# Kernel tuning notes

Hardware: AMD Instinct MI355X
Metric: run time of the kernel (lower is better)

The kernel has to match this reference:

```python
import jax, jax.numpy as jnp
import numpy as np

N_NODES = 50000
N_EDGES = 800000
D_IN = 128
D_HID = 128
D_OUT = 128


def _graph_conv(x, src, dst, ew, w_rel, w_root, b):
    # PyG GraphConv: out_i = (sum_{j->i} ew_ji * x_j) @ w_rel.T + b + x_i @ w_root.T
    msg = x[src] * ew[:, None]                                   # [E, F] gather + scale
    agg = jax.ops.segment_sum(msg, dst, num_segments=x.shape[0])  # [N, F] scatter-add
    return agg @ w_rel.T + x @ w_root.T + b


def setup_inputs() -> dict:
    key = jax.random.key(0)
    ks = jax.random.split(key, 12)
    s = 0.05
    x = jax.random.normal(ks[0], (N_NODES, D_IN), dtype=jnp.float32)
    edge_index = jax.random.randint(ks[1], (2, N_EDGES), 0, N_NODES, dtype=jnp.int32)
    edge_weight = jax.random.uniform(ks[2], (N_EDGES,), dtype=jnp.float32)
    return {
        "x": x,
        "edge_index": edge_index,
        "edge_weight": edge_weight,
        "w1_rel": jax.random.normal(ks[3], (D_HID, D_IN), dtype=jnp.float32) * s,
        "w1_root": jax.random.normal(ks[4], (D_HID, D_IN), dtype=jnp.float32) * s,
        "b1": jnp.zeros((D_HID,), dtype=jnp.float32),
        "w2_rel": jax.random.normal(ks[5], (D_HID, D_HID), dtype=jnp.float32) * s,
        "w2_root": jax.random.normal(ks[6], (D_HID, D_HID), dtype=jnp.float32) * s,
        "b2": jnp.zeros((D_HID,), dtype=jnp.float32),
        "w3_rel": jax.random.normal(ks[7], (D_OUT, D_HID), dtype=jnp.float32) * s,
        "w3_root": jax.random.normal(ks[8], (D_OUT, D_HID), dtype=jnp.float32) * s,
        "b3": jnp.zeros((D_OUT,), dtype=jnp.float32),
    }


def reference(x, edge_index, edge_weight,
              w1_rel, w1_root, b1,
              w2_rel, w2_root, b2,
              w3_rel, w3_root, b3):
    src, dst = edge_index[0], edge_index[1]
    h = _graph_conv(x, src, dst, edge_weight, w1_rel, w1_root, b1)
    h = jax.nn.relu(h)  # dropout is identity in eval mode
    h = _graph_conv(h, src, dst, edge_weight, w2_rel, w2_root, b2)
    h = jax.nn.relu(h)
    out = _graph_conv(h, src, dst, edge_weight, w3_rel, w3_root, b3)
    return out
```

## Files before the change

kernel.cpp:

```cpp
#include <hip/hip_runtime.h>
#include <hip/hip_bf16.h>

#define DFEAT   128
#define BCAP    2048
#define NB_MAX  1024

typedef __attribute__((ext_vector_type(8))) short bf16x8;
typedef __attribute__((ext_vector_type(4))) float f32x4;
typedef unsigned int uint;


__global__ __launch_bounds__(1024) void bin_scatter(const int* __restrict__ src,
                                                    const int* __restrict__ dst,
                                                    const float* __restrict__ ew,
                                                    int* __restrict__ cursor,
                                                    int2* __restrict__ bedges,
                                                    int E, int NB) {
    __shared__ int hist[NB_MAX];
    __shared__ int base[NB_MAX];
    const int tid = threadIdx.x;
    for (int b = tid; b < NB; b += 1024) hist[b] = 0;
    __syncthreads();

    int  s[8]; float w[8]; int bk[8]; int dl[8];
    const int i0 = blockIdx.x * 8192 + tid;
    #pragma unroll
    for (int k = 0; k < 8; ++k) {
        int i = i0 + k * 1024;
        if (i < E) {
            s[k] = src[i]; w[k] = ew[i];
            int d = dst[i];
            bk[k] = d >> 6; dl[k] = d & 63;
            atomicAdd(&hist[bk[k]], 1);
        } else bk[k] = -1;
    }
    __syncthreads();
    for (int b = tid; b < NB; b += 1024) {
        int c = hist[b];
        base[b] = (c > 0) ? atomicAdd(&cursor[b], c) : 0;
        hist[b] = 0;
    }
    __syncthreads();
    #pragma unroll
    for (int k = 0; k < 8; ++k) {
        if (bk[k] >= 0) {
            int r = atomicAdd(&hist[bk[k]], 1);
            int pos = base[bk[k]] + r;
            if (pos < ((bk[k] + 1) << 11)) {
                bedges[pos] = make_int2(s[k] | (dl[k] << 26), __float_as_int(w[k]));
            }
        }
    }
}


__global__ __launch_bounds__(1024) void bucket_sort(const int* __restrict__ cursor,
                                                    int2* __restrict__ bedges,
                                                    int* __restrict__ rowptr,
                                                    int* __restrict__ rowend, int N) {
    __shared__ int2 buf[BCAP];
    __shared__ int hist[64], pref[64], rank[64];
    const int b = blockIdx.x, tid = threadIdx.x;
    const int base = b << 11;
    const int cnt = cursor[b] - base;

    if (tid < 64) hist[tid] = 0;
    __syncthreads();
    for (int i = tid; i < cnt; i += 1024) {
        int2 e = bedges[base + i];
        buf[i] = e;
        atomicAdd(&hist[((uint)e.x) >> 26], 1);
    }
    __syncthreads();
    if (tid < 64) {
        int v = hist[tid];
        int s = v;
        #pragma unroll
        for (int off = 1; off < 64; off <<= 1) {
            int t = __shfl_up(s, off, 64);
            if (tid >= off) s += t;
        }
        pref[tid] = s - v;
        rank[tid] = 0;
        int node = b * 64 + tid;
        if (node < N) {
            rowptr[node] = base + (s - v);
            rowend[node] = base + s;
        }
    }
    __syncthreads();
    for (int i = tid; i < cnt; i += 1024) {
        int2 e = buf[i];
        int dl = ((uint)e.x) >> 26;
        int r = atomicAdd(&rank[dl], 1);
        bedges[base + pref[dl] + r] = e;
    }
}


__device__ __forceinline__ uint pack_bf16x2(float a, float b) {
    __hip_bfloat16 ba = __float2bfloat16(a);
    __hip_bfloat16 bb = __float2bfloat16(b);
    unsigned short ua = *(unsigned short*)&ba;
    unsigned short ub = *(unsigned short*)&bb;
    return (uint)ua | ((uint)ub << 16);
}


__global__ void prep_all(const float* __restrict__ x, uint* __restrict__ xb, int n2,
                         const float* __restrict__ w1r, const float* __restrict__ w1t,
                         const float* __restrict__ w2r, const float* __restrict__ w2t,
                         const float* __restrict__ w3r, const float* __restrict__ w3t,
                         __hip_bfloat16* __restrict__ Bp1, __hip_bfloat16* __restrict__ Bp2,
                         __hip_bfloat16* __restrict__ Bp3,
                         int* __restrict__ cursor, int NB, int cvtB) {
    const int b = blockIdx.x, tid = threadIdx.x;
    if (b < cvtB) {
        int i = b * 256 + tid;
        if (i < n2) {
            float2 v = ((const float2*)x)[i];
            xb[i] = pack_bf16x2(v.x, v.y);
        }
    } else if (b < cvtB + 384) {
        const int b2 = b - cvtB;
        const int g = b2 >> 7;
        const int idx = (b2 & 127) * 256 + tid;
        const float* wrel  = (g == 0) ? w1r : (g == 1) ? w2r : w3r;
        const float* wroot = (g == 0) ? w1t : (g == 1) ? w2t : w3t;
        __hip_bfloat16* Bp = (g == 0) ? Bp1 : (g == 1) ? Bp2 : Bp3;
        int j     = idx & 7;
        int lane  = (idx >> 3) & 63;
        int nfrag = (idx >> 9) & 7;
        int kstep = idx >> 12;
        int k = kstep * 32 + (lane >> 4) * 8 + j;
        int n = nfrag * 16 + (lane & 15);
        float v = (k < 128) ? wrel[n * 128 + k] : wroot[n * 128 + (k - 128)];
        Bp[idx] = __float2bfloat16(v);
    } else {
        int i = (b - cvtB - 384) * 256 + tid;
        if (i < NB) cursor[i] = i * BCAP;
    }
}


template<int RELU, int OUTF32>
__global__ __launch_bounds__(512) void fused_layer(const uint* __restrict__ f,
                                                   const int* __restrict__ rowptr,
                                                   const int* __restrict__ rowend,
                                                   const int2* __restrict__ bedges,
                                                   const bf16x8* __restrict__ Bp,
                                                   const float* __restrict__ bias,
                                                   float* __restrict__ outf,
                                                   __hip_bfloat16* __restrict__ outb,
                                                   int N) {
    __shared__ uint4 As4[64][17];
    const int tid  = threadIdx.x;
    const int lane = tid & 63, wid = tid >> 6;
    const int grp  = lane >> 4;
    const int sub  = lane & 15;
    const int tile = blockIdx.x * 64;
    const uint4* f4 = (const uint4*)f;

    const int pn = tile + wid * 8 + (lane & 7);
    int rp = 0, re = 0;
    if (lane < 8 && pn < N) { rp = rowptr[pn]; re = rowend[pn]; }

    for (int q = 0; q < 8; ++q) {
        const int node = tile + wid * 8 + q;
        const int beg = __builtin_amdgcn_readlane(rp, q);
        const int end = __builtin_amdgcn_readlane(re, q);
        const int deg = end - beg;

        float acc[8];
        #pragma unroll
        for (int i = 0; i < 8; ++i) acc[i] = 0.f;

        if (node < N) {
            int done = 0;
            while (done < deg) {
                const int chunk = min(deg - done, 64);
                int2 e = bedges[beg + done + min(lane, chunk - 1)];
                const int vsrc = e.x & 0x03FFFFFF;
                const int vwb  = (lane < chunk) ? e.y : 0;
                const int iters = (chunk + 7) & ~7;
                for (int j = 0; j < iters; j += 8) {
                    const int   s0 = __shfl(vsrc, j + grp, 64);
                    const float w0 = __int_as_float(__shfl(vwb, j + grp, 64));
                    const int   s1 = __shfl(vsrc, j + 4 + grp, 64);
                    const float w1 = __int_as_float(__shfl(vwb, j + 4 + grp, 64));
                    const uint4 q0 = f4[(size_t)s0 * 16 + sub];
                    const uint4 q1 = f4[(size_t)s1 * 16 + sub];
                    acc[0] = fmaf(w0, __uint_as_float(q0.x << 16),         acc[0]);
                    acc[1] = fmaf(w0, __uint_as_float(q0.x & 0xffff0000u), acc[1]);
                    acc[2] = fmaf(w0, __uint_as_float(q0.y << 16),         acc[2]);
                    acc[3] = fmaf(w0, __uint_as_float(q0.y & 0xffff0000u), acc[3]);
                    acc[4] = fmaf(w0, __uint_as_float(q0.z << 16),         acc[4]);
                    acc[5] = fmaf(w0, __uint_as_float(q0.z & 0xffff0000u), acc[5]);
                    acc[6] = fmaf(w0, __uint_as_float(q0.w << 16),         acc[6]);
                    acc[7] = fmaf(w0, __uint_as_float(q0.w & 0xffff0000u), acc[7]);
                    acc[0] = fmaf(w1, __uint_as_float(q1.x << 16),         acc[0]);
                    acc[1] = fmaf(w1, __uint_as_float(q1.x & 0xffff0000u), acc[1]);
                    acc[2] = fmaf(w1, __uint_as_float(q1.y << 16),         acc[2]);
                    acc[3] = fmaf(w1, __uint_as_float(q1.y & 0xffff0000u), acc[3]);
                    acc[4] = fmaf(w1, __uint_as_float(q1.z << 16),         acc[4]);
                    acc[5] = fmaf(w1, __uint_as_float(q1.z & 0xffff0000u), acc[5]);
                    acc[6] = fmaf(w1, __uint_as_float(q1.w << 16),         acc[6]);
                    acc[7] = fmaf(w1, __uint_as_float(q1.w & 0xffff0000u), acc[7]);
                }
                done += chunk;
            }
        }
        #pragma unroll
        for (int i = 0; i < 8; ++i) {
            acc[i] += __shfl_xor(acc[i], 16, 64);
            acc[i] += __shfl_xor(acc[i], 32, 64);
        }
        if (lane < 16) {
            uint4 o;
            o.x = pack_bf16x2(acc[0], acc[1]);
            o.y = pack_bf16x2(acc[2], acc[3]);
            o.z = pack_bf16x2(acc[4], acc[5]);
            o.w = pack_bf16x2(acc[6], acc[7]);
            As4[wid * 8 + q][sub] = o;
        }
    }
    __syncthreads();

    const int wr = wid >> 2, wc = wid & 3;
    const int lrow = lane & 15;
    const int lkq  = (lane >> 4);
    const short* As_s = (const short*)&As4[0][0];
    const short* fb   = (const short*)f;

    int grow[2];
    #pragma unroll
    for (int mi = 0; mi < 2; ++mi) {
        int r = tile + wr * 32 + mi * 16 + lrow;
        grow[mi] = (r < N) ? r : (N - 1);
    }

    f32x4 acc2[2][2];
    #pragma unroll
    for (int mi = 0; mi < 2; ++mi)
        #pragma unroll
        for (int nf = 0; nf < 2; ++nf) acc2[mi][nf] = (f32x4){0.f, 0.f, 0.f, 0.f};

    #pragma unroll
    for (int ks = 0; ks < 8; ++ks) {
        bf16x8 a[2], b[2];
        #pragma unroll
        for (int mi = 0; mi < 2; ++mi) {
            if (ks < 4)
                a[mi] = *(const bf16x8*)(As_s + (wr * 32 + mi * 16 + lrow) * 136 + ks * 32 + lkq * 8);
            else
                a[mi] = *(const bf16x8*)(fb + (size_t)grow[mi] * 128 + (ks - 4) * 32 + lkq * 8);
        }
        #pragma unroll
        for (int nf = 0; nf < 2; ++nf)
            b[nf] = Bp[(ks * 8 + (wc * 2 + nf)) * 64 + lane];
        #pragma unroll
        for (int mi = 0; mi < 2; ++mi)
            #pragma unroll
            for (int nf = 0; nf < 2; ++nf)
                acc2[mi][nf] = __builtin_amdgcn_mfma_f32_16x16x32_bf16(a[mi], b[nf], acc2[mi][nf], 0, 0, 0);
    }

    const int crow = (lane >> 4) * 4;
    const int ccol = lane & 15;
    #pragma unroll
    for (int mi = 0; mi < 2; ++mi) {
        #pragma unroll
        for (int nf = 0; nf < 2; ++nf) {
            const int col = wc * 32 + nf * 16 + ccol;
            const float bv = bias[col];
            #pragma unroll
            for (int r = 0; r < 4; ++r) {
                const int row = tile + wr * 32 + mi * 16 + crow + r;
                if (row < N) {
                    float v = acc2[mi][nf][r] + bv;
                    if (RELU) v = fmaxf(v, 0.f);
                    if (OUTF32) outf[(size_t)row * 128 + col] = v;
                    else        outb[(size_t)row * 128 + col] = __float2bfloat16(v);
                }
            }
        }
    }
}


extern "C" void kernel_launch(void* const* d_in, const int* in_sizes, int n_in,
                              void* d_out, int out_size, void* d_ws, size_t ws_size,
                              hipStream_t stream) {
    const float* x   = (const float*)d_in[0];
    const int*  eidx = (const int*)d_in[1];
    const float* ew  = (const float*)d_in[2];
    const float* w1r = (const float*)d_in[3];
    const float* w1t = (const float*)d_in[4];
    const float* b1  = (const float*)d_in[5];
    const float* w2r = (const float*)d_in[6];
    const float* w2t = (const float*)d_in[7];
    const float* b2  = (const float*)d_in[8];
    const float* w3r = (const float*)d_in[9];
    const float* w3t = (const float*)d_in[10];
    const float* b3  = (const float*)d_in[11];
    float* out = (float*)d_out;

    const int N  = in_sizes[0] / DFEAT;
    const int E  = in_sizes[2];
    const int NB = (N + 63) / 64;

    char* ws = (char*)d_ws;
    size_t off = 0;
    auto alloc = [&](size_t bytes) -> void* {
        off = (off + 255) & ~(size_t)255;
        void* p = ws + off;
        off += bytes;
        return p;
    };
    int*  cursor = (int*)alloc((size_t)NB * 4);
    int*  rowptr = (int*)alloc((size_t)N * 4);
    int*  rowend = (int*)alloc((size_t)N * 4);
    int2* bedges = (int2*)alloc((size_t)NB * BCAP * 8);
    __hip_bfloat16* Bp1 = (__hip_bfloat16*)alloc(32768 * 2);
    __hip_bfloat16* Bp2 = (__hip_bfloat16*)alloc(32768 * 2);
    __hip_bfloat16* Bp3 = (__hip_bfloat16*)alloc(32768 * 2);
    uint* xb   = (uint*)alloc((size_t)N * 64 * 4);
    uint* h1b  = (uint*)alloc((size_t)N * 64 * 4);
    uint* h2b  = (uint*)alloc((size_t)N * 64 * 4);
    (void)ws_size;

    const int* src = eidx;
    const int* dst = eidx + E;

    const int n2 = N * 64;
    const int cvtB = (n2 + 255) / 256;
    const int curB = (NB + 255) / 256;
    prep_all<<<cvtB + 384 + curB, 256, 0, stream>>>(x, xb, n2,
                                                    w1r, w1t, w2r, w2t, w3r, w3t,
                                                    Bp1, Bp2, Bp3, cursor, NB, cvtB);

    bin_scatter<<<(E + 8191) / 8192, 1024, 0, stream>>>(src, dst, ew, cursor, bedges, E, NB);
    bucket_sort<<<NB, 1024, 0, stream>>>(cursor, bedges, rowptr, rowend, N);

    fused_layer<1, 0><<<NB, 512, 0, stream>>>(xb, rowptr, rowend, bedges, (const bf16x8*)Bp1,
                                              b1, nullptr, (__hip_bfloat16*)h1b, N);
    fused_layer<1, 0><<<NB, 512, 0, stream>>>(h1b, rowptr, rowend, bedges, (const bf16x8*)Bp2,
                                              b2, nullptr, (__hip_bfloat16*)h2b, N);
    fused_layer<0, 1><<<NB, 512, 0, stream>>>(h2b, rowptr, rowend, bedges, (const bf16x8*)Bp3,
                                              b3, out, nullptr, N);
}
```

Before: 152.2 us.

## Halve node tile per block and software-pipeline edge and feature gathers

Each fused_layer block now handles 32 nodes instead of 64, giving 4 nodes per wave and twice as many blocks for better load balance and occupancy. The edge list for the next node is prefetched while the current node aggregates. Inside the aggregation loop the feature gathers for the next 8 edges are issued before the FMAs of the current ones. The MFMA stage shrinks to one 16-row tile per wave, so per-block weight loads are amortised over fewer rows.

```diff
diff --git a/kernel.cpp b/kernel.cpp
--- a/kernel.cpp
+++ b/kernel.cpp
@@ -104,6 +104,17 @@
     unsigned short ua = *(unsigned short*)&ba;
     unsigned short ub = *(unsigned short*)&bb;
     return (uint)ua | ((uint)ub << 16);
+}
+
+__device__ __forceinline__ void fma8(float* acc, uint4 q, float wt) {
+    acc[0] = fmaf(wt, __uint_as_float(q.x << 16),         acc[0]);
+    acc[1] = fmaf(wt, __uint_as_float(q.x & 0xffff0000u), acc[1]);
+    acc[2] = fmaf(wt, __uint_as_float(q.y << 16),         acc[2]);
+    acc[3] = fmaf(wt, __uint_as_float(q.y & 0xffff0000u), acc[3]);
+    acc[4] = fmaf(wt, __uint_as_float(q.z << 16),         acc[4]);
+    acc[5] = fmaf(wt, __uint_as_float(q.z & 0xffff0000u), acc[5]);
+    acc[6] = fmaf(wt, __uint_as_float(q.w << 16),         acc[6]);
+    acc[7] = fmaf(wt, __uint_as_float(q.w & 0xffff0000u), acc[7]);
 }
 
 
@@ -153,63 +164,64 @@
                                                    float* __restrict__ outf,
                                                    __hip_bfloat16* __restrict__ outb,
                                                    int N) {
-    __shared__ uint4 As4[64][17];
+    __shared__ uint4 As4[32][17];
     const int tid  = threadIdx.x;
     const int lane = tid & 63, wid = tid >> 6;
     const int grp  = lane >> 4;
     const int sub  = lane & 15;
-    const int tile = blockIdx.x * 64;
+    const int tile = blockIdx.x * 32;
     const uint4* f4 = (const uint4*)f;
 
-    const int pn = tile + wid * 8 + (lane & 7);
+    const int pn = tile + wid * 4 + (lane & 3);
     int rp = 0, re = 0;
-    if (lane < 8 && pn < N) { rp = rowptr[pn]; re = rowend[pn]; }
-
-    for (int q = 0; q < 8; ++q) {
-        const int node = tile + wid * 8 + q;
-        const int beg = __builtin_amdgcn_readlane(rp, q);
-        const int end = __builtin_amdgcn_readlane(re, q);
-        const int deg = end - beg;
+    if (lane < 4 && pn < N) { rp = rowptr[pn]; re = rowend[pn]; }
+
+    int begC = __builtin_amdgcn_readlane(rp, 0);
+    int degC = __builtin_amdgcn_readlane(re, 0) - begC;
+    int2 eCur = make_int2(0, 0);
+    if (degC > 0) eCur = bedges[begC + min(lane, min(degC, 64) - 1)];
+
+    for (int qn = 0; qn < 4; ++qn) {
+        const int beg = begC, deg = degC;
+        int2 eNext = make_int2(0, 0);
+        if (qn < 3) {
+            begC = __builtin_amdgcn_readlane(rp, qn + 1);
+            degC = __builtin_amdgcn_readlane(re, qn + 1) - begC;
+            if (degC > 0) eNext = bedges[begC + min(lane, min(degC, 64) - 1)];
+        }
 
         float acc[8];
         #pragma unroll
         for (int i = 0; i < 8; ++i) acc[i] = 0.f;
 
-        if (node < N) {
-            int done = 0;
-            while (done < deg) {
-                const int chunk = min(deg - done, 64);
-                int2 e = bedges[beg + done + min(lane, chunk - 1)];
-                const int vsrc = e.x & 0x03FFFFFF;
-                const int vwb  = (lane < chunk) ? e.y : 0;
-                const int iters = (chunk + 7) & ~7;
-                for (int j = 0; j < iters; j += 8) {
-                    const int   s0 = __shfl(vsrc, j + grp, 64);
-                    const float w0 = __int_as_float(__shfl(vwb, j + grp, 64));
-                    const int   s1 = __shfl(vsrc, j + 4 + grp, 64);
-                    const float w1 = __int_as_float(__shfl(vwb, j + 4 + grp, 64));
-                    const uint4 q0 = f4[(size_t)s0 * 16 + sub];
-                    const uint4 q1 = f4[(size_t)s1 * 16 + sub];
-                    acc[0] = fmaf(w0, __uint_as_float(q0.x << 16),         acc[0]);
-                    acc[1] = fmaf(w0, __uint_as_float(q0.x & 0xffff0000u), acc[1]);
-                    acc[2] = fmaf(w0, __uint_as_float(q0.y << 16),         acc[2]);
-                    acc[3] = fmaf(w0, __uint_as_float(q0.y & 0xffff0000u), acc[3]);
-                    acc[4] = fmaf(w0, __uint_as_float(q0.z << 16),         acc[4]);
-                    acc[5] = fmaf(w0, __uint_as_float(q0.z & 0xffff0000u), acc[5]);
-                    acc[6] = fmaf(w0, __uint_as_float(q0.w << 16),         acc[6]);
-                    acc[7] = fmaf(w0, __uint_as_float(q0.w & 0xffff0000u), acc[7]);
-                    acc[0] = fmaf(w1, __uint_as_float(q1.x << 16),         acc[0]);
-                    acc[1] = fmaf(w1, __uint_as_float(q1.x & 0xffff0000u), acc[1]);
-                    acc[2] = fmaf(w1, __uint_as_float(q1.y << 16),         acc[2]);
-                    acc[3] = fmaf(w1, __uint_as_float(q1.y & 0xffff0000u), acc[3]);
-                    acc[4] = fmaf(w1, __uint_as_float(q1.z << 16),         acc[4]);
-                    acc[5] = fmaf(w1, __uint_as_float(q1.z & 0xffff0000u), acc[5]);
-                    acc[6] = fmaf(w1, __uint_as_float(q1.w << 16),         acc[6]);
-                    acc[7] = fmaf(w1, __uint_as_float(q1.w & 0xffff0000u), acc[7]);
-                }
-                done += chunk;
+        int done = 0;
+        int2 e = eCur;
+        while (done < deg) {
+            const int chunk = min(deg - done, 64);
+            if (done) e = bedges[beg + done + min(lane, chunk - 1)];
+            const int vsrc = e.x & 0x03FFFFFF;
+            const int vwb  = (lane < chunk) ? e.y : 0;
+            const int iters = (chunk + 7) & ~7;
+            int   s0 = __shfl(vsrc, grp, 64);
+            float w0 = __int_as_float(__shfl(vwb, grp, 64));
+            int   s1 = __shfl(vsrc, 4 + grp, 64);
+            float w1 = __int_as_float(__shfl(vwb, 4 + grp, 64));
+            uint4 q0 = f4[(size_t)s0 * 16 + sub];
+            uint4 q1 = f4[(size_t)s1 * 16 + sub];
+            for (int j = 8; j < iters; j += 8) {
+                int   s2 = __shfl(vsrc, j + grp, 64);
+                float w2 = __int_as_float(__shfl(vwb, j + grp, 64));
+                int   s3 = __shfl(vsrc, j + 4 + grp, 64);
+                float w3 = __int_as_float(__shfl(vwb, j + 4 + grp, 64));
+                uint4 q2 = f4[(size_t)s2 * 16 + sub];
+                uint4 q3 = f4[(size_t)s3 * 16 + sub];
+                fma8(acc, q0, w0); fma8(acc, q1, w1);
+                q0 = q2; q1 = q3; w0 = w2; w1 = w3;
             }
-        }
+            fma8(acc, q0, w0); fma8(acc, q1, w1);
+            done += chunk;
+        }
+
         #pragma unroll
         for (int i = 0; i < 8; ++i) {
             acc[i] += __shfl_xor(acc[i], 16, 64);
@@ -221,8 +233,9 @@
             o.y = pack_bf16x2(acc[2], acc[3]);
             o.z = pack_bf16x2(acc[4], acc[5]);
             o.w = pack_bf16x2(acc[6], acc[7]);
-            As4[wid * 8 + q][sub] = o;
-        }
+            As4[wid * 4 + qn][sub] = o;
+        }
+        eCur = eNext;
     }
     __syncthreads();
 
@@ -232,56 +245,41 @@
     const short* As_s = (const short*)&As4[0][0];
     const short* fb   = (const short*)f;
 
-    int grow[2];
-    #pragma unroll
-    for (int mi = 0; mi < 2; ++mi) {
-        int r = tile + wr * 32 + mi * 16 + lrow;
-        grow[mi] = (r < N) ? r : (N - 1);
-    }
-
-    f32x4 acc2[2][2];
-    #pragma unroll
-    for (int mi = 0; mi < 2; ++mi)
-        #pragma unroll
-        for (int nf = 0; nf < 2; ++nf) acc2[mi][nf] = (f32x4){0.f, 0.f, 0.f, 0.f};
+    int gr = tile + wr * 16 + lrow;
+    if (gr >= N) gr = N - 1;
+
+    f32x4 acc2[2];
+    acc2[0] = (f32x4){0.f, 0.f, 0.f, 0.f};
+    acc2[1] = (f32x4){0.f, 0.f, 0.f, 0.f};
 
     #pragma unroll
     for (int ks = 0; ks < 8; ++ks) {
-        bf16x8 a[2], b[2];
-        #pragma unroll
-        for (int mi = 0; mi < 2; ++mi) {
-            if (ks < 4)
-                a[mi] = *(const bf16x8*)(As_s + (wr * 32 + mi * 16 + lrow) * 136 + ks * 32 + lkq * 8);
-            else
-                a[mi] = *(const bf16x8*)(fb + (size_t)grow[mi] * 128 + (ks - 4) * 32 + lkq * 8);
-        }
-        #pragma unroll
-        for (int nf = 0; nf < 2; ++nf)
-            b[nf] = Bp[(ks * 8 + (wc * 2 + nf)) * 64 + lane];
-        #pragma unroll
-        for (int mi = 0; mi < 2; ++mi)
-            #pragma unroll
-            for (int nf = 0; nf < 2; ++nf)
-                acc2[mi][nf] = __builtin_amdgcn_mfma_f32_16x16x32_bf16(a[mi], b[nf], acc2[mi][nf], 0, 0, 0);
+        bf16x8 a;
+        if (ks < 4)
+            a = *(const bf16x8*)(As_s + (wr * 16 + lrow) * 136 + ks * 32 + lkq * 8);
+        else
+            a = *(const bf16x8*)(fb + (size_t)gr * 128 + (ks - 4) * 32 + lkq * 8);
+        #pragma unroll
+        for (int nf = 0; nf < 2; ++nf) {
+            bf16x8 b = Bp[(ks * 8 + (wc * 2 + nf)) * 64 + lane];
+            acc2[nf] = __builtin_amdgcn_mfma_f32_16x16x32_bf16(a, b, acc2[nf], 0, 0, 0);
+        }
     }
 
     const int crow = (lane >> 4) * 4;
     const int ccol = lane & 15;
     #pragma unroll
-    for (int mi = 0; mi < 2; ++mi) {
-        #pragma unroll
-        for (int nf = 0; nf < 2; ++nf) {
-            const int col = wc * 32 + nf * 16 + ccol;
-            const float bv = bias[col];
-            #pragma unroll
-            for (int r = 0; r < 4; ++r) {
-                const int row = tile + wr * 32 + mi * 16 + crow + r;
-                if (row < N) {
-                    float v = acc2[mi][nf][r] + bv;
-                    if (RELU) v = fmaxf(v, 0.f);
-                    if (OUTF32) outf[(size_t)row * 128 + col] = v;
-                    else        outb[(size_t)row * 128 + col] = __float2bfloat16(v);
-                }
+    for (int nf = 0; nf < 2; ++nf) {
+        const int col = wc * 32 + nf * 16 + ccol;
+        const float bv = bias[col];
+        #pragma unroll
+        for (int r = 0; r < 4; ++r) {
+            const int row = tile + wr * 16 + crow + r;
+            if (row < N) {
+                float v = acc2[nf][r] + bv;
+                if (RELU) v = fmaxf(v, 0.f);
+                if (OUTF32) outf[(size_t)row * 128 + col] = v;
+                else        outb[(size_t)row * 128 + col] = __float2bfloat16(v);
             }
         }
     }
@@ -342,10 +340,11 @@
     bin_scatter<<<(E + 8191) / 8192, 1024, 0, stream>>>(src, dst, ew, cursor, bedges, E, NB);
     bucket_sort<<<NB, 1024, 0, stream>>>(cursor, bedges, rowptr, rowend, N);
 
-    fused_layer<1, 0><<<NB, 512, 0, stream>>>(xb, rowptr, rowend, bedges, (const bf16x8*)Bp1,
-                                              b1, nullptr, (__hip_bfloat16*)h1b, N);
-    fused_layer<1, 0><<<NB, 512, 0, stream>>>(h1b, rowptr, rowend, bedges, (const bf16x8*)Bp2,
-                                              b2, nullptr, (__hip_bfloat16*)h2b, N);
-    fused_layer<0, 1><<<NB, 512, 0, stream>>>(h2b, rowptr, rowend, bedges, (const bf16x8*)Bp3,
-                                              b3, out, nullptr, N);
-}
+    const int NB2 = (N + 31) / 32;
+    fused_layer<1, 0><<<NB2, 512, 0, stream>>>(xb, rowptr, rowend, bedges, (const bf16x8*)Bp1,
+                                               b1, nullptr, (__hip_bfloat16*)h1b, N);
+    fused_layer<1, 0><<<NB2, 512, 0, stream>>>(h1b, rowptr, rowend, bedges, (const bf16x8*)Bp2,
+                                               b2, nullptr, (__hip_bfloat16*)h2b, N);
+    fused_layer<0, 1><<<NB2, 512, 0, stream>>>(h2b, rowptr, rowend, bedges, (const bf16x8*)Bp3,
+                                               b3, out, nullptr, N);
+}
```

Result: slower. 156.3 us (+2.7%).

## Split aggregation into feature-slice kernel and separate node GEMM kernel

Applied to the files above, without the earlier changes.

Breaks each fused layer into two kernels. A slice_agg kernel gives each block one of four 32-feature slices, so each lane gathers a single uint per edge, which is meant to make the gathered working set of each pass fit in cache. The aggregate is written to a sliced bf16 buffer that a separate MFMA GEMM kernel then reads. This adds a global round trip for the aggregate, extra launches, and fourfold re-reading of the edge lists, in exchange for better cache locality and more parallel blocks.

```diff
diff --git a/kernel.cpp b/kernel.cpp
--- a/kernel.cpp
+++ b/kernel.cpp
@@ -143,94 +143,75 @@
 }
 
 
-template<int RELU, int OUTF32>
-__global__ __launch_bounds__(512) void fused_layer(const uint* __restrict__ f,
-                                                   const int* __restrict__ rowptr,
-                                                   const int* __restrict__ rowend,
-                                                   const int2* __restrict__ bedges,
-                                                   const bf16x8* __restrict__ Bp,
-                                                   const float* __restrict__ bias,
-                                                   float* __restrict__ outf,
-                                                   __hip_bfloat16* __restrict__ outb,
-                                                   int N) {
-    __shared__ uint4 As4[64][17];
-    const int tid  = threadIdx.x;
-    const int lane = tid & 63, wid = tid >> 6;
-    const int grp  = lane >> 4;
-    const int sub  = lane & 15;
-    const int tile = blockIdx.x * 64;
-    const uint4* f4 = (const uint4*)f;
-
-    const int pn = tile + wid * 8 + (lane & 7);
+__global__ __launch_bounds__(256) void slice_agg(const uint* __restrict__ f,
+                                                 const int* __restrict__ rowptr,
+                                                 const int* __restrict__ rowend,
+                                                 const int2* __restrict__ bedges,
+                                                 uint* __restrict__ aggS, int N) {
+    const int p   = blockIdx.x & 3;
+    const int b   = blockIdx.x >> 2;
+    const int lane = threadIdx.x & 63, wid = threadIdx.x >> 6;
+    const int grp = lane >> 4;
+    const int sub = lane & 15;
+    const int tile = b * 64;
+    const uint* fp = f + p * 16;
+
+    const int pn = tile + wid * 16 + (lane & 15);
     int rp = 0, re = 0;
-    if (lane < 8 && pn < N) { rp = rowptr[pn]; re = rowend[pn]; }
-
-    for (int q = 0; q < 8; ++q) {
-        const int node = tile + wid * 8 + q;
+    if (lane < 16 && pn < N) { rp = rowptr[pn]; re = rowend[pn]; }
+
+    for (int q = 0; q < 16; ++q) {
+        const int node = tile + wid * 16 + q;
         const int beg = __builtin_amdgcn_readlane(rp, q);
-        const int end = __builtin_amdgcn_readlane(re, q);
-        const int deg = end - beg;
-
-        float acc[8];
-        #pragma unroll
-        for (int i = 0; i < 8; ++i) acc[i] = 0.f;
-
-        if (node < N) {
+        const int deg = __builtin_amdgcn_readlane(re, q) - beg;
+
+        float a0 = 0.f, a1 = 0.f;
+        if (node < N && deg > 0) {
             int done = 0;
             while (done < deg) {
                 const int chunk = min(deg - done, 64);
                 int2 e = bedges[beg + done + min(lane, chunk - 1)];
                 const int vsrc = e.x & 0x03FFFFFF;
                 const int vwb  = (lane < chunk) ? e.y : 0;
-                const int iters = (chunk + 7) & ~7;
-                for (int j = 0; j < iters; j += 8) {
-                    const int   s0 = __shfl(vsrc, j + grp, 64);
-                    const float w0 = __int_as_float(__shfl(vwb, j + grp, 64));
-                    const int   s1 = __shfl(vsrc, j + 4 + grp, 64);
-                    const float w1 = __int_as_float(__shfl(vwb, j + 4 + grp, 64));
-                    const uint4 q0 = f4[(size_t)s0 * 16 + sub];
-                    const uint4 q1 = f4[(size_t)s1 * 16 + sub];
-                    acc[0] = fmaf(w0, __uint_as_float(q0.x << 16),         acc[0]);
-                    acc[1] = fmaf(w0, __uint_as_float(q0.x & 0xffff0000u), acc[1]);
-                    acc[2] = fmaf(w0, __uint_as_float(q0.y << 16),         acc[2]);
-                    acc[3] = fmaf(w0, __uint_as_float(q0.y & 0xffff0000u), acc[3]);
-                    acc[4] = fmaf(w0, __uint_as_float(q0.z << 16),         acc[4]);
-                    acc[5] = fmaf(w0, __uint_as_float(q0.z & 0xffff0000u), acc[5]);
-                    acc[6] = fmaf(w0, __uint_as_float(q0.w << 16),         acc[6]);
-                    acc[7] = fmaf(w0, __uint_as_float(q0.w & 0xffff0000u), acc[7]);
-                    acc[0] = fmaf(w1, __uint_as_float(q1.x << 16),         acc[0]);
-                    acc[1] = fmaf(w1, __uint_as_float(q1.x & 0xffff0000u), acc[1]);
-                    acc[2] = fmaf(w1, __uint_as_float(q1.y << 16),         acc[2]);
-                    acc[3] = fmaf(w1, __uint_as_float(q1.y & 0xffff0000u), acc[3]);
-                    acc[4] = fmaf(w1, __uint_as_float(q1.z << 16),         acc[4]);
-                    acc[5] = fmaf(w1, __uint_as_float(q1.z & 0xffff0000u), acc[5]);
-                    acc[6] = fmaf(w1, __uint_as_float(q1.w << 16),         acc[6]);
-                    acc[7] = fmaf(w1, __uint_as_float(q1.w & 0xffff0000u), acc[7]);
+                const int iters = (chunk + 3) & ~3;
+                int   s0 = __shfl(vsrc, grp, 64);
+                float w0 = __int_as_float(__shfl(vwb, grp, 64));
+                uint  v0 = fp[(size_t)s0 * 64 + sub];
+                for (int j = 4; j < iters; j += 4) {
+                    int   s1 = __shfl(vsrc, j + grp, 64);
+                    float w1 = __int_as_float(__shfl(vwb, j + grp, 64));
+                    uint  v1 = fp[(size_t)s1 * 64 + sub];
+                    a0 = fmaf(w0, __uint_as_float(v0 << 16),         a0);
+                    a1 = fmaf(w0, __uint_as_float(v0 & 0xffff0000u), a1);
+                    v0 = v1; w0 = w1;
                 }
+                a0 = fmaf(w0, __uint_as_float(v0 << 16),         a0);
+                a1 = fmaf(w0, __uint_as_float(v0 & 0xffff0000u), a1);
                 done += chunk;
             }
         }
-        #pragma unroll
-        for (int i = 0; i < 8; ++i) {
-            acc[i] += __shfl_xor(acc[i], 16, 64);
-            acc[i] += __shfl_xor(acc[i], 32, 64);
-        }
-        if (lane < 16) {
-            uint4 o;
-            o.x = pack_bf16x2(acc[0], acc[1]);
-            o.y = pack_bf16x2(acc[2], acc[3]);
-            o.z = pack_bf16x2(acc[4], acc[5]);
-            o.w = pack_bf16x2(acc[6], acc[7]);
-            As4[wid * 8 + q][sub] = o;
-        }
-    }
-    __syncthreads();
-
+        a0 += __shfl_xor(a0, 16, 64); a0 += __shfl_xor(a0, 32, 64);
+        a1 += __shfl_xor(a1, 16, 64); a1 += __shfl_xor(a1, 32, 64);
+        if (lane < 16 && node < N)
+            aggS[((size_t)p * N + node) * 16 + sub] = pack_bf16x2(a0, a1);
+    }
+}
+
+
+template<int RELU, int OUTF32>
+__global__ __launch_bounds__(512) void gemm_node(const uint* __restrict__ aggS,
+                                                 const uint* __restrict__ f,
+                                                 const bf16x8* __restrict__ Bp,
+                                                 const float* __restrict__ bias,
+                                                 float* __restrict__ outf,
+                                                 __hip_bfloat16* __restrict__ outb,
+                                                 int N) {
+    const int lane = threadIdx.x & 63, wid = threadIdx.x >> 6;
     const int wr = wid >> 2, wc = wid & 3;
+    const int tile = blockIdx.x * 64;
     const int lrow = lane & 15;
-    const int lkq  = (lane >> 4);
-    const short* As_s = (const short*)&As4[0][0];
-    const short* fb   = (const short*)f;
+    const int lkq  = lane >> 4;
+    const short* fb = (const short*)f;
 
     int grow[2];
     #pragma unroll
@@ -250,10 +231,14 @@
         bf16x8 a[2], b[2];
         #pragma unroll
         for (int mi = 0; mi < 2; ++mi) {
-            if (ks < 4)
-                a[mi] = *(const bf16x8*)(As_s + (wr * 32 + mi * 16 + lrow) * 136 + ks * 32 + lkq * 8);
-            else
+            if (ks < 4) {
+                const int cb = ks * 32 + lkq * 8;
+                const int pc = cb >> 5;
+                const int uo = (cb & 31) >> 1;
+                a[mi] = *(const bf16x8*)(aggS + ((size_t)pc * N + grow[mi]) * 16 + uo);
+            } else {
                 a[mi] = *(const bf16x8*)(fb + (size_t)grow[mi] * 128 + (ks - 4) * 32 + lkq * 8);
+            }
         }
         #pragma unroll
         for (int nf = 0; nf < 2; ++nf)
@@ -325,6 +310,7 @@
     __hip_bfloat16* Bp2 = (__hip_bfloat16*)alloc(32768 * 2);
     __hip_bfloat16* Bp3 = (__hip_bfloat16*)alloc(32768 * 2);
     uint* xb   = (uint*)alloc((size_t)N * 64 * 4);
+    uint* aggS = (uint*)alloc((size_t)4 * N * 16 * 4);
     uint* h1b  = (uint*)alloc((size_t)N * 64 * 4);
     uint* h2b  = (uint*)alloc((size_t)N * 64 * 4);
     (void)ws_size;
@@ -342,10 +328,13 @@
     bin_scatter<<<(E + 8191) / 8192, 1024, 0, stream>>>(src, dst, ew, cursor, bedges, E, NB);
     bucket_sort<<<NB, 1024, 0, stream>>>(cursor, bedges, rowptr, rowend, N);
 
-    fused_layer<1, 0><<<NB, 512, 0, stream>>>(xb, rowptr, rowend, bedges, (const bf16x8*)Bp1,
-                                              b1, nullptr, (__hip_bfloat16*)h1b, N);
-    fused_layer<1, 0><<<NB, 512, 0, stream>>>(h1b, rowptr, rowend, bedges, (const bf16x8*)Bp2,
-                                              b2, nullptr, (__hip_bfloat16*)h2b, N);
-    fused_layer<0, 1><<<NB, 512, 0, stream>>>(h2b, rowptr, rowend, bedges, (const bf16x8*)Bp3,
-                                              b3, out, nullptr, N);
-}
+    slice_agg<<<NB * 4, 256, 0, stream>>>(xb, rowptr, rowend, bedges, aggS, N);
+    gemm_node<1, 0><<<NB, 512, 0, stream>>>(aggS, xb, (const bf16x8*)Bp1,
+                                            b1, nullptr, (__hip_bfloat16*)h1b, N);
+    slice_agg<<<NB * 4, 256, 0, stream>>>(h1b, rowptr, rowend, bedges, aggS, N);
+    gemm_node<1, 0><<<NB, 512, 0, stream>>>(aggS, h1b, (const bf16x8*)Bp2,
+                                            b2, nullptr, (__hip_bfloat16*)h2b, N);
+    slice_agg<<<NB * 4, 256, 0, stream>>>(h2b, rowptr, rowend, bedges, aggS, N);
+    gemm_node<0, 1><<<NB, 512, 0, stream>>>(aggS, h2b, (const bf16x8*)Bp3,
+                                            b3, out, nullptr, N);
+}
```

After: 315.3 us. +107.1%, slower.
